# Kernel tuning notes

Hardware: AMD Instinct MI355X
Metric: run time of the kernel (lower is better)

Reference implementation:

```python
import jax, jax.numpy as jnp
import numpy as np

N_II = 100000      # item nodes
N_UIU = 200000     # user + item nodes
D = 64             # embedding_dim
E_II = 600000
E_UIU = 1200000
L_II = 3           # num_layers_ii
L_UIU = 3          # num_layers_uiu
N_USERS = 100000   # items occupy indices [N_USERS, N_USERS+N_II)


def _lightgcn_embedding(x, edge_index, edge_weight, num_layers, num_nodes):
    """PyG LightGCN.get_embedding: symmetric gcn_norm (no self loops) + mean over layer outputs."""
    src, dst = edge_index[0], edge_index[1]
    # gcn_norm: deg over target nodes, weighted by edge_weight
    deg = jax.ops.segment_sum(edge_weight, dst, num_segments=num_nodes)
    deg_inv_sqrt = jnp.where(deg > 0, jax.lax.rsqrt(jnp.where(deg > 0, deg, 1.0)), 0.0)
    norm = deg_inv_sqrt[src] * edge_weight * deg_inv_sqrt[dst]  # [E]
    alpha = 1.0 / (num_layers + 1)
    out = x * alpha
    for _ in range(num_layers):
        # SpMM: gather source embeddings, scale, scatter-add to targets
        x = jax.ops.segment_sum(norm[:, None] * x[src], dst, num_segments=num_nodes)  # [N, D]
        out = out + x * alpha
    return out


def setup_inputs() -> dict:
    key = jax.random.key(0)
    k1, k2, k3, k4, k5, k6 = jax.random.split(key, 6)
    return {
        "emb_ii": jax.random.normal(k1, (N_II, D), dtype=jnp.float32),
        "emb_uiu": jax.random.normal(k2, (N_UIU, D), dtype=jnp.float32),
        "edge_attr_ii": jax.random.uniform(k3, (E_II,), dtype=jnp.float32),
        "edge_attr_uiu": jax.random.uniform(k4, (E_UIU,), dtype=jnp.float32),
        "edge_index_ii": jax.random.randint(k5, (2, E_II), 0, N_II, dtype=jnp.int32),
        "edge_index_uiu": jax.random.randint(k6, (2, E_UIU), 0, N_UIU, dtype=jnp.int32),
        # contiguous item block starting at N_USERS (node_mask_item.nonzero())
        "item_idx": jnp.arange(N_II, dtype=jnp.int32) + N_USERS,
    }


def reference(emb_ii, emb_uiu, edge_attr_ii, edge_attr_uiu,
              edge_index_ii, edge_index_uiu, item_idx):
    # item-item graph propagation
    h_ii = _lightgcn_embedding(emb_ii, edge_index_ii, edge_attr_ii, L_II, N_II)  # [N_II, D]
    # write item embeddings into the user-item embedding table
    emb_uiu = emb_uiu.at[item_idx].set(h_ii)
    # user-item graph propagation
    h_uiu = _lightgcn_embedding(emb_uiu, edge_index_uiu, edge_attr_uiu, L_UIU, N_UIU)  # [N_UIU, D]
    return h_uiu
```

## Files before the change

### kernel.cpp

```cpp
#include <hip/hip_runtime.h>


#define D       64
#define N_II    100000
#define N_UIU   200000
#define E_II    600000
#define E_UIU   1200000
#define N_USERS 100000

__device__ __forceinline__ unsigned short f2bf(float f) {
    unsigned u = __float_as_uint(f);
    u += 0x7fffu + ((u >> 16) & 1u);
    return (unsigned short)(u >> 16);
}
__device__ __forceinline__ void bf8_fma(float acc[8], uint4 p, float v) {
    acc[0] += v * __uint_as_float(p.x << 16);
    acc[1] += v * __uint_as_float(p.x & 0xffff0000u);
    acc[2] += v * __uint_as_float(p.y << 16);
    acc[3] += v * __uint_as_float(p.y & 0xffff0000u);
    acc[4] += v * __uint_as_float(p.z << 16);
    acc[5] += v * __uint_as_float(p.z & 0xffff0000u);
    acc[6] += v * __uint_as_float(p.w << 16);
    acc[7] += v * __uint_as_float(p.w & 0xffff0000u);
}
__device__ __forceinline__ void bf8_add(float acc[8], uint4 p) {
    acc[0] += __uint_as_float(p.x << 16);
    acc[1] += __uint_as_float(p.x & 0xffff0000u);
    acc[2] += __uint_as_float(p.y << 16);
    acc[3] += __uint_as_float(p.y & 0xffff0000u);
    acc[4] += __uint_as_float(p.z << 16);
    acc[5] += __uint_as_float(p.z & 0xffff0000u);
    acc[6] += __uint_as_float(p.w << 16);
    acc[7] += __uint_as_float(p.w & 0xffff0000u);
}
__device__ __forceinline__ uint4 pack8(const float a[8]) {
    uint4 r;
    r.x = (unsigned)f2bf(a[0]) | ((unsigned)f2bf(a[1]) << 16);
    r.y = (unsigned)f2bf(a[2]) | ((unsigned)f2bf(a[3]) << 16);
    r.z = (unsigned)f2bf(a[4]) | ((unsigned)f2bf(a[5]) << 16);
    r.w = (unsigned)f2bf(a[6]) | ((unsigned)f2bf(a[7]) << 16);
    return r;
}


__global__ void k_cnt_rank(const int* __restrict__ dst, int* __restrict__ cnt,
                           int* __restrict__ rank, int E) {
    int e = blockIdx.x * blockDim.x + threadIdx.x;
    if (e < E) rank[e] = atomicAdd(&cnt[dst[e]], 1);
}

__global__ void k_blkred(const int* __restrict__ cnt, int* __restrict__ blk, int N) {
    __shared__ int sh[256];
    int i = blockIdx.x * 256 + threadIdx.x;
    sh[threadIdx.x] = (i < N) ? cnt[i] : 0;
    __syncthreads();
    for (int s = 128; s > 0; s >>= 1) {
        if (threadIdx.x < s) sh[threadIdx.x] += sh[threadIdx.x + s];
        __syncthreads();
    }
    if (threadIdx.x == 0) blk[blockIdx.x] = sh[0];
}

__global__ void k_blkscan(int* __restrict__ blk, int nb) {
    __shared__ int sh[1024];
    int t = threadIdx.x;
    sh[t] = (t < nb) ? blk[t] : 0;
    __syncthreads();
    for (int off = 1; off < 1024; off <<= 1) {
        int v = (t >= off) ? sh[t - off] : 0;
        __syncthreads();
        sh[t] += v;
        __syncthreads();
    }
    if (t < nb) blk[t] = (t > 0) ? sh[t - 1] : 0;
}

__global__ void k_rowoff(const int* __restrict__ cnt, const int* __restrict__ blk,
                         int* __restrict__ roff, int* __restrict__ rend, int N) {
    __shared__ int sh[256];
    int t = threadIdx.x;
    int i = blockIdx.x * 256 + t;
    int v = (i < N) ? cnt[i] : 0;
    sh[t] = v;
    __syncthreads();
    for (int off = 1; off < 256; off <<= 1) {
        int u = (t >= off) ? sh[t - off] : 0;
        __syncthreads();
        sh[t] += u;
        __syncthreads();
    }
    if (i < N) {
        int o = blk[blockIdx.x] + sh[t] - v;
        roff[i] = o;
        rend[i] = o + v;
    }
}

__global__ void k_fillE(const int* __restrict__ src, const int* __restrict__ dst,
                        const float* __restrict__ w, const int* __restrict__ rank,
                        const int* __restrict__ roff, int* __restrict__ csrc,
                        float* __restrict__ cw, int E) {
    int e = blockIdx.x * blockDim.x + threadIdx.x;
    if (e < E) {
        int pos = roff[dst[e]] + rank[e];
        csrc[pos] = src[e];
        cw[pos]   = w[e];
    }
}

__global__ void k_deg_dis(const int* __restrict__ roff, const int* __restrict__ rend,
                          const float* __restrict__ cw, float* __restrict__ dis, int N) {
    int i = blockIdx.x * blockDim.x + threadIdx.x;
    if (i >= N) return;
    float dg = 0.f;
    for (int j = roff[i]; j < rend[i]; ++j) dg += cw[j];
    dis[i] = (dg > 0.f) ? rsqrtf(dg) : 0.f;
}

__global__ void k_val(const int* __restrict__ roff, const int* __restrict__ rend,
                      const int* __restrict__ csrc, const float* __restrict__ dis,
                      float* __restrict__ cval, int N) {
    int i = blockIdx.x * blockDim.x + threadIdx.x;
    if (i >= N) return;
    float di = dis[i];
    for (int j = roff[i]; j < rend[i]; ++j)
        cval[j] = di * cval[j] * dis[csrc[j]];
}

__global__ void k_cvt(const float4* __restrict__ x, uint4* __restrict__ xb, int n8) {
    int i = blockIdx.x * blockDim.x + threadIdx.x;
    if (i >= n8) return;
    float4 a = x[2 * i], b = x[2 * i + 1];
    float t[8] = {a.x, a.y, a.z, a.w, b.x, b.y, b.z, b.w};
    xb[i] = pack8(t);
}

__global__ void k_spmm8(const int* __restrict__ roff, const int* __restrict__ rend,
                        const int* __restrict__ csrc, const float* __restrict__ cval,
                        const uint4* __restrict__ xb, uint4* __restrict__ xn, int N) {
    int idx = blockIdx.x * blockDim.x + threadIdx.x;
    int row = idx >> 3;
    if (row >= N) return;
    int g = idx & 7;
    int s = roff[row], e = rend[row];
    float acc[8] = {0.f, 0.f, 0.f, 0.f, 0.f, 0.f, 0.f, 0.f};
    int j = s;
    for (; j + 1 < e; j += 2) {
        int   s0 = csrc[j],   s1 = csrc[j + 1];
        float v0 = cval[j],   v1 = cval[j + 1];
        uint4 a0 = xb[s0 * 8 + g];
        uint4 a1 = xb[s1 * 8 + g];
        bf8_fma(acc, a0, v0);
        bf8_fma(acc, a1, v1);
    }
    if (j < e) {
        uint4 a0 = xb[csrc[j] * 8 + g];
        bf8_fma(acc, a0, cval[j]);
    }
    xn[row * 8 + g] = pack8(acc);
}

__global__ void k_spmm8_final(const int* __restrict__ roff, const int* __restrict__ rend,
                              const int* __restrict__ csrc, const float* __restrict__ cval,
                              const uint4* __restrict__ x2b, const uint4* __restrict__ x1b,
                              const float4* __restrict__ x0, float4* __restrict__ out,
                              float alpha, int N) {
    int idx = blockIdx.x * blockDim.x + threadIdx.x;
    int row = idx >> 3;
    if (row >= N) return;
    int g = idx & 7;
    int s = roff[row], e = rend[row];
    float acc[8] = {0.f, 0.f, 0.f, 0.f, 0.f, 0.f, 0.f, 0.f};
    int j = s;
    for (; j + 1 < e; j += 2) {
        int   s0 = csrc[j],   s1 = csrc[j + 1];
        float v0 = cval[j],   v1 = cval[j + 1];
        uint4 a0 = x2b[s0 * 8 + g];
        uint4 a1 = x2b[s1 * 8 + g];
        bf8_fma(acc, a0, v0);
        bf8_fma(acc, a1, v1);
    }
    if (j < e) {
        uint4 a0 = x2b[csrc[j] * 8 + g];
        bf8_fma(acc, a0, cval[j]);
    }
    bf8_add(acc, x1b[row * 8 + g]);
    bf8_add(acc, x2b[row * 8 + g]);
    float4 b0 = x0[row * 16 + 2 * g];
    float4 b1 = x0[row * 16 + 2 * g + 1];
    out[row * 16 + 2 * g] = make_float4(alpha * (b0.x + acc[0]), alpha * (b0.y + acc[1]),
                                        alpha * (b0.z + acc[2]), alpha * (b0.w + acc[3]));
    out[row * 16 + 2 * g + 1] = make_float4(alpha * (b1.x + acc[4]), alpha * (b1.y + acc[5]),
                                            alpha * (b1.z + acc[6]), alpha * (b1.w + acc[7]));
}


static void run_graph(const int* src, const int* dst, const float* w, int E, int N,
                      const float* x0, float* out,
                      uint4* xb0, uint4* x1, uint4* x2,
                      int* csrc, float* cval, int* rank, int* cnt,
                      int* roff, int* rend, float* dis, int* blk,
                      hipStream_t stream) {
    const int B = 256;
    const int nbE = (E + B - 1) / B;
    const int nbN = (N + B - 1) / B;
    const float alpha = 0.25f;

    hipMemsetAsync(cnt, 0, (size_t)N * sizeof(int), stream);
    k_cnt_rank<<<nbE, B, 0, stream>>>(dst, cnt, rank, E);
    k_blkred  <<<nbN, B, 0, stream>>>(cnt, blk, N);
    k_blkscan <<<1, 1024, 0, stream>>>(blk, nbN);
    k_rowoff  <<<nbN, B, 0, stream>>>(cnt, blk, roff, rend, N);
    k_fillE   <<<nbE, B, 0, stream>>>(src, dst, w, rank, roff, csrc, cval, E);
    k_deg_dis <<<nbN, B, 0, stream>>>(roff, rend, cval, dis, N);
    k_val     <<<nbN, B, 0, stream>>>(roff, rend, csrc, dis, cval, N);

    const int n8 = N * 8;
    const int ng = (n8 + B - 1) / B;
    k_cvt<<<ng, B, 0, stream>>>((const float4*)x0, xb0, n8);
    k_spmm8<<<ng, B, 0, stream>>>(roff, rend, csrc, cval, xb0, x1, N);
    k_spmm8<<<ng, B, 0, stream>>>(roff, rend, csrc, cval, x1, x2, N);
    k_spmm8_final<<<ng, B, 0, stream>>>(roff, rend, csrc, cval, x2, x1,
                                        (const float4*)x0, (float4*)out, alpha, N);
}

extern "C" void kernel_launch(void* const* d_in, const int* in_sizes, int n_in,
                              void* d_out, int out_size, void* d_ws, size_t ws_size,
                              hipStream_t stream) {
    const float* emb_ii  = (const float*)d_in[0];
    float*       emb_uiu = (float*)d_in[1];
    const float* w_ii    = (const float*)d_in[2];
    const float* w_uiu   = (const float*)d_in[3];
    const int*   src_ii  = (const int*)d_in[4];
    const int*   dst_ii  = src_ii + E_II;
    const int*   src_uiu = (const int*)d_in[5];
    const int*   dst_uiu = src_uiu + E_UIU;
    float*       out     = (float*)d_out;

    uint4* xb0  = (uint4*)d_ws;
    uint4* x1   = xb0 + (size_t)N_UIU * 8;
    uint4* x2   = x1 + (size_t)N_UIU * 8;
    int*   csrc = (int*)(x2 + (size_t)N_UIU * 8);
    float* cval = (float*)(csrc + E_UIU);
    int*   rank = (int*)(cval + E_UIU);
    int*   cnt  = rank + E_UIU;
    int*   roff = cnt + N_UIU;
    int*   rend = roff + N_UIU;
    float* dis  = (float*)(rend + N_UIU);
    int*   blk  = (int*)(dis + N_UIU);

    float* hii = emb_uiu + (size_t)N_USERS * D;
    run_graph(src_ii, dst_ii, w_ii, E_II, N_II, emb_ii, hii,
              xb0, x1, x2, csrc, cval, rank, cnt, roff, rend, dis, blk, stream);

    run_graph(src_uiu, dst_uiu, w_uiu, E_UIU, N_UIU, emb_uiu, out,
              xb0, x1, x2, csrc, cval, rank, cnt, roff, rend, dis, blk, stream);
}
```

Baseline: 504.6 us.

## Pack CSR edges as int2, use atomic-base scan, fuse bf16 writeback of item embeddings

CSR source indices and edge values are interleaved into one int2 array, so each edge needs a single 8-byte load in the SpMM and preprocessing kernels. The three-kernel block reduce/scan/offset sequence becomes one kernel that claims its block base with an atomicAdd on a global cursor. This yields valid but non-deterministically ordered CSR row placement, and it drops two launches. The item-graph final kernel also writes the bf16 copy of its output straight into the user-item input buffer, so the second conversion covers only the user rows.

After: 488.2 us. 1.03x faster.

```diff
diff --git a/kernel.cpp b/kernel.cpp
--- a/kernel.cpp
+++ b/kernel.cpp
@@ -49,35 +49,10 @@
     if (e < E) rank[e] = atomicAdd(&cnt[dst[e]], 1);
 }
 
-__global__ void k_blkred(const int* __restrict__ cnt, int* __restrict__ blk, int N) {
+__global__ void k_rowoff(const int* __restrict__ cnt, int* __restrict__ roff,
+                         int* __restrict__ rend, int* __restrict__ gcur, int N) {
     __shared__ int sh[256];
-    int i = blockIdx.x * 256 + threadIdx.x;
-    sh[threadIdx.x] = (i < N) ? cnt[i] : 0;
-    __syncthreads();
-    for (int s = 128; s > 0; s >>= 1) {
-        if (threadIdx.x < s) sh[threadIdx.x] += sh[threadIdx.x + s];
-        __syncthreads();
-    }
-    if (threadIdx.x == 0) blk[blockIdx.x] = sh[0];
-}
-
-__global__ void k_blkscan(int* __restrict__ blk, int nb) {
-    __shared__ int sh[1024];
-    int t = threadIdx.x;
-    sh[t] = (t < nb) ? blk[t] : 0;
-    __syncthreads();
-    for (int off = 1; off < 1024; off <<= 1) {
-        int v = (t >= off) ? sh[t - off] : 0;
-        __syncthreads();
-        sh[t] += v;
-        __syncthreads();
-    }
-    if (t < nb) blk[t] = (t > 0) ? sh[t - 1] : 0;
-}
-
-__global__ void k_rowoff(const int* __restrict__ cnt, const int* __restrict__ blk,
-                         int* __restrict__ roff, int* __restrict__ rend, int N) {
-    __shared__ int sh[256];
+    __shared__ int base;
     int t = threadIdx.x;
     int i = blockIdx.x * 256 + t;
     int v = (i < N) ? cnt[i] : 0;
@@ -89,8 +64,10 @@
         sh[t] += u;
         __syncthreads();
     }
+    if (t == 255) base = atomicAdd(gcur, sh[255]);
+    __syncthreads();
     if (i < N) {
-        int o = blk[blockIdx.x] + sh[t] - v;
+        int o = base + sh[t] - v;
         roff[i] = o;
         rend[i] = o + v;
     }
@@ -98,33 +75,32 @@
 
 __global__ void k_fillE(const int* __restrict__ src, const int* __restrict__ dst,
                         const float* __restrict__ w, const int* __restrict__ rank,
-                        const int* __restrict__ roff, int* __restrict__ csrc,
-                        float* __restrict__ cw, int E) {
+                        const int* __restrict__ roff, int2* __restrict__ ev, int E) {
     int e = blockIdx.x * blockDim.x + threadIdx.x;
     if (e < E) {
         int pos = roff[dst[e]] + rank[e];
-        csrc[pos] = src[e];
-        cw[pos]   = w[e];
+        ev[pos] = make_int2(src[e], __float_as_int(w[e]));
     }
 }
 
 __global__ void k_deg_dis(const int* __restrict__ roff, const int* __restrict__ rend,
-                          const float* __restrict__ cw, float* __restrict__ dis, int N) {
+                          const int2* __restrict__ ev, float* __restrict__ dis, int N) {
     int i = blockIdx.x * blockDim.x + threadIdx.x;
     if (i >= N) return;
     float dg = 0.f;
-    for (int j = roff[i]; j < rend[i]; ++j) dg += cw[j];
+    for (int j = roff[i]; j < rend[i]; ++j) dg += __int_as_float(ev[j].y);
     dis[i] = (dg > 0.f) ? rsqrtf(dg) : 0.f;
 }
 
 __global__ void k_val(const int* __restrict__ roff, const int* __restrict__ rend,
-                      const int* __restrict__ csrc, const float* __restrict__ dis,
-                      float* __restrict__ cval, int N) {
+                      const float* __restrict__ dis, int2* __restrict__ ev, int N) {
     int i = blockIdx.x * blockDim.x + threadIdx.x;
     if (i >= N) return;
     float di = dis[i];
-    for (int j = roff[i]; j < rend[i]; ++j)
-        cval[j] = di * cval[j] * dis[csrc[j]];
+    for (int j = roff[i]; j < rend[i]; ++j) {
+        int2 p = ev[j];
+        ev[j].y = __float_as_int(di * __int_as_float(p.y) * dis[p.x]);
+    }
 }
 
 __global__ void k_cvt(const float4* __restrict__ x, uint4* __restrict__ xb, int n8) {
@@ -136,8 +112,8 @@
 }
 
 __global__ void k_spmm8(const int* __restrict__ roff, const int* __restrict__ rend,
-                        const int* __restrict__ csrc, const float* __restrict__ cval,
-                        const uint4* __restrict__ xb, uint4* __restrict__ xn, int N) {
+                        const int2* __restrict__ ev, const uint4* __restrict__ xb,
+                        uint4* __restrict__ xn, int N) {
     int idx = blockIdx.x * blockDim.x + threadIdx.x;
     int row = idx >> 3;
     if (row >= N) return;
@@ -146,24 +122,24 @@
     float acc[8] = {0.f, 0.f, 0.f, 0.f, 0.f, 0.f, 0.f, 0.f};
     int j = s;
     for (; j + 1 < e; j += 2) {
-        int   s0 = csrc[j],   s1 = csrc[j + 1];
-        float v0 = cval[j],   v1 = cval[j + 1];
-        uint4 a0 = xb[s0 * 8 + g];
-        uint4 a1 = xb[s1 * 8 + g];
-        bf8_fma(acc, a0, v0);
-        bf8_fma(acc, a1, v1);
+        int2 p0 = ev[j], p1 = ev[j + 1];
+        uint4 a0 = xb[p0.x * 8 + g];
+        uint4 a1 = xb[p1.x * 8 + g];
+        bf8_fma(acc, a0, __int_as_float(p0.y));
+        bf8_fma(acc, a1, __int_as_float(p1.y));
     }
     if (j < e) {
-        uint4 a0 = xb[csrc[j] * 8 + g];
-        bf8_fma(acc, a0, cval[j]);
+        int2 p0 = ev[j];
+        uint4 a0 = xb[p0.x * 8 + g];
+        bf8_fma(acc, a0, __int_as_float(p0.y));
     }
     xn[row * 8 + g] = pack8(acc);
 }
 
 __global__ void k_spmm8_final(const int* __restrict__ roff, const int* __restrict__ rend,
-                              const int* __restrict__ csrc, const float* __restrict__ cval,
-                              const uint4* __restrict__ x2b, const uint4* __restrict__ x1b,
-                              const float4* __restrict__ x0, float4* __restrict__ out,
+                              const int2* __restrict__ ev, const uint4* __restrict__ x2b,
+                              const uint4* __restrict__ x1b, const float4* __restrict__ x0,
+                              float4* __restrict__ out, uint4* __restrict__ outb,
                               float alpha, int N) {
     int idx = blockIdx.x * blockDim.x + threadIdx.x;
     int row = idx >> 3;
@@ -173,55 +149,44 @@
     float acc[8] = {0.f, 0.f, 0.f, 0.f, 0.f, 0.f, 0.f, 0.f};
     int j = s;
     for (; j + 1 < e; j += 2) {
-        int   s0 = csrc[j],   s1 = csrc[j + 1];
-        float v0 = cval[j],   v1 = cval[j + 1];
-        uint4 a0 = x2b[s0 * 8 + g];
-        uint4 a1 = x2b[s1 * 8 + g];
-        bf8_fma(acc, a0, v0);
-        bf8_fma(acc, a1, v1);
+        int2 p0 = ev[j], p1 = ev[j + 1];
+        uint4 a0 = x2b[p0.x * 8 + g];
+        uint4 a1 = x2b[p1.x * 8 + g];
+        bf8_fma(acc, a0, __int_as_float(p0.y));
+        bf8_fma(acc, a1, __int_as_float(p1.y));
     }
     if (j < e) {
-        uint4 a0 = x2b[csrc[j] * 8 + g];
-        bf8_fma(acc, a0, cval[j]);
+        int2 p0 = ev[j];
+        uint4 a0 = x2b[p0.x * 8 + g];
+        bf8_fma(acc, a0, __int_as_float(p0.y));
     }
     bf8_add(acc, x1b[row * 8 + g]);
     bf8_add(acc, x2b[row * 8 + g]);
     float4 b0 = x0[row * 16 + 2 * g];
     float4 b1 = x0[row * 16 + 2 * g + 1];
-    out[row * 16 + 2 * g] = make_float4(alpha * (b0.x + acc[0]), alpha * (b0.y + acc[1]),
-                                        alpha * (b0.z + acc[2]), alpha * (b0.w + acc[3]));
-    out[row * 16 + 2 * g + 1] = make_float4(alpha * (b1.x + acc[4]), alpha * (b1.y + acc[5]),
-                                            alpha * (b1.z + acc[6]), alpha * (b1.w + acc[7]));
-}
-
-
-static void run_graph(const int* src, const int* dst, const float* w, int E, int N,
-                      const float* x0, float* out,
-                      uint4* xb0, uint4* x1, uint4* x2,
-                      int* csrc, float* cval, int* rank, int* cnt,
-                      int* roff, int* rend, float* dis, int* blk,
-                      hipStream_t stream) {
+    float r[8] = {alpha * (b0.x + acc[0]), alpha * (b0.y + acc[1]),
+                  alpha * (b0.z + acc[2]), alpha * (b0.w + acc[3]),
+                  alpha * (b1.x + acc[4]), alpha * (b1.y + acc[5]),
+                  alpha * (b1.z + acc[6]), alpha * (b1.w + acc[7])};
+    out[row * 16 + 2 * g]     = make_float4(r[0], r[1], r[2], r[3]);
+    out[row * 16 + 2 * g + 1] = make_float4(r[4], r[5], r[6], r[7]);
+    if (outb) outb[row * 8 + g] = pack8(r);
+}
+
+
+static void build_csr(const int* src, const int* dst, const float* w, int E, int N,
+                      int2* ev, int* rank, int* cnt, int* roff, int* rend,
+                      float* dis, hipStream_t stream) {
     const int B = 256;
     const int nbE = (E + B - 1) / B;
     const int nbN = (N + B - 1) / B;
-    const float alpha = 0.25f;
-
-    hipMemsetAsync(cnt, 0, (size_t)N * sizeof(int), stream);
+    int* gcur = cnt + N;
+    hipMemsetAsync(cnt, 0, ((size_t)N + 1) * sizeof(int), stream);
     k_cnt_rank<<<nbE, B, 0, stream>>>(dst, cnt, rank, E);
-    k_blkred  <<<nbN, B, 0, stream>>>(cnt, blk, N);
-    k_blkscan <<<1, 1024, 0, stream>>>(blk, nbN);
-    k_rowoff  <<<nbN, B, 0, stream>>>(cnt, blk, roff, rend, N);
-    k_fillE   <<<nbE, B, 0, stream>>>(src, dst, w, rank, roff, csrc, cval, E);
-    k_deg_dis <<<nbN, B, 0, stream>>>(roff, rend, cval, dis, N);
-    k_val     <<<nbN, B, 0, stream>>>(roff, rend, csrc, dis, cval, N);
-
-    const int n8 = N * 8;
-    const int ng = (n8 + B - 1) / B;
-    k_cvt<<<ng, B, 0, stream>>>((const float4*)x0, xb0, n8);
-    k_spmm8<<<ng, B, 0, stream>>>(roff, rend, csrc, cval, xb0, x1, N);
-    k_spmm8<<<ng, B, 0, stream>>>(roff, rend, csrc, cval, x1, x2, N);
-    k_spmm8_final<<<ng, B, 0, stream>>>(roff, rend, csrc, cval, x2, x1,
-                                        (const float4*)x0, (float4*)out, alpha, N);
+    k_rowoff  <<<nbN, B, 0, stream>>>(cnt, roff, rend, gcur, N);
+    k_fillE   <<<nbE, B, 0, stream>>>(src, dst, w, rank, roff, ev, E);
+    k_deg_dis <<<nbN, B, 0, stream>>>(roff, rend, ev, dis, N);
+    k_val     <<<nbN, B, 0, stream>>>(roff, rend, dis, ev, N);
 }
 
 extern "C" void kernel_launch(void* const* d_in, const int* in_sizes, int n_in,
@@ -237,22 +202,47 @@
     const int*   dst_uiu = src_uiu + E_UIU;
     float*       out     = (float*)d_out;
 
-    uint4* xb0  = (uint4*)d_ws;
-    uint4* x1   = xb0 + (size_t)N_UIU * 8;
-    uint4* x2   = x1 + (size_t)N_UIU * 8;
-    int*   csrc = (int*)(x2 + (size_t)N_UIU * 8);
-    float* cval = (float*)(csrc + E_UIU);
-    int*   rank = (int*)(cval + E_UIU);
-    int*   cnt  = rank + E_UIU;
-    int*   roff = cnt + N_UIU;
-    int*   rend = roff + N_UIU;
-    float* dis  = (float*)(rend + N_UIU);
-    int*   blk  = (int*)(dis + N_UIU);
-
-    float* hii = emb_uiu + (size_t)N_USERS * D;
-    run_graph(src_ii, dst_ii, w_ii, E_II, N_II, emb_ii, hii,
-              xb0, x1, x2, csrc, cval, rank, cnt, roff, rend, dis, blk, stream);
-
-    run_graph(src_uiu, dst_uiu, w_uiu, E_UIU, N_UIU, emb_uiu, out,
-              xb0, x1, x2, csrc, cval, rank, cnt, roff, rend, dis, blk, stream);
-}
+    uint4* xb0_u = (uint4*)d_ws;
+    uint4* x1_u  = xb0_u + (size_t)N_UIU * 8;
+    uint4* x2_u  = x1_u + (size_t)N_UIU * 8;
+    int2*  ev    = (int2*)(x2_u + (size_t)N_UIU * 8);
+    int*   rank  = (int*)(ev + E_UIU);
+    int*   cnt   = rank + E_UIU;
+    int*   roff  = cnt + N_UIU + 1;
+    int*   rend  = roff + N_UIU;
+    float* dis   = (float*)(rend + N_UIU);
+
+    uint4* g1_x0 = x1_u;
+    uint4* g1_x1 = x1_u + (size_t)N_II * 8;
+    uint4* g1_x2 = x2_u;
+
+    const int B = 256;
+    const float alpha = 0.25f;
+
+    build_csr(src_ii, dst_ii, w_ii, E_II, N_II, ev, rank, cnt, roff, rend, dis, stream);
+    {
+        const int n8 = N_II * 8;
+        const int ng = (n8 + B - 1) / B;
+        float* hii = emb_uiu + (size_t)N_USERS * D;
+        uint4* hii_b = xb0_u + (size_t)N_USERS * 8;
+        k_cvt  <<<ng, B, 0, stream>>>((const float4*)emb_ii, g1_x0, n8);
+        k_spmm8<<<ng, B, 0, stream>>>(roff, rend, ev, g1_x0, g1_x1, N_II);
+        k_spmm8<<<ng, B, 0, stream>>>(roff, rend, ev, g1_x1, g1_x2, N_II);
+        k_spmm8_final<<<ng, B, 0, stream>>>(roff, rend, ev, g1_x2, g1_x1,
+                                            (const float4*)emb_ii, (float4*)hii, hii_b,
+                                            alpha, N_II);
+    }
+
+    build_csr(src_uiu, dst_uiu, w_uiu, E_UIU, N_UIU, ev, rank, cnt, roff, rend, dis, stream);
+    {
+        const int n8u = N_USERS * 8;
+        k_cvt<<<(n8u + B - 1) / B, B, 0, stream>>>((const float4*)emb_uiu, xb0_u, n8u);
+        const int n8 = N_UIU * 8;
+        const int ng = (n8 + B - 1) / B;
+        k_spmm8<<<ng, B, 0, stream>>>(roff, rend, ev, xb0_u, x1_u, N_UIU);
+        k_spmm8<<<ng, B, 0, stream>>>(roff, rend, ev, x1_u, x2_u, N_UIU);
+        k_spmm8_final<<<ng, B, 0, stream>>>(roff, rend, ev, x2_u, x1_u,
+                                            (const float4*)emb_uiu, (float4*)out, nullptr,
+                                            alpha, N_UIU);
+    }
+}
```
